# Performance work log

Hardware: AMD Instinct MI355X
Metric: run time of the kernel (lower is better)

The kernel has to match this reference:

```python
import jax, jax.numpy as jnp
import numpy as np

N = 50000   # nodes
E = 640000  # edges (before self-loops)
D = 128     # in_dim == out_dim
H = 4       # heads
C = 32      # per-head channels (out_dim // heads)
ED = 1      # edge_dim
NEG_SLOPE = 0.2
LN_EPS = 1e-5


def setup_inputs() -> dict:
    key = jax.random.key(0)
    ks = jax.random.split(key, 8)
    glorot = lambda k, sh, fan: jax.random.normal(k, sh, jnp.float32) / np.float32(np.sqrt(fan))
    return dict(
        x=jax.random.normal(ks[0], (N, D), jnp.float32),
        edge_index=jax.random.randint(ks[1], (2, E), 0, N, dtype=jnp.int32),
        edge_attr=jax.random.uniform(ks[2], (E, ED), jnp.float32),
        W_l=glorot(ks[3], (D, H * C), D), b_l=jnp.zeros((H * C,), jnp.float32),
        W_r=glorot(ks[4], (D, H * C), D), b_r=jnp.zeros((H * C,), jnp.float32),
        W_e=glorot(ks[5], (ED, H * C), ED),
        att=glorot(ks[6], (H, C), C),
        bias=jnp.zeros((H * C,), jnp.float32),
        ln_gamma=jnp.ones((H * C,), jnp.float32),
        ln_beta=jnp.zeros((H * C,), jnp.float32),
    )


def reference(x, edge_index, edge_attr, W_l, b_l, W_r, b_r, W_e, att, bias, ln_gamma, ln_beta):
    n = x.shape[0]
    src, dst = edge_index[0], edge_index[1]
    # --- add self loops; self-loop edge_attr = mean of incoming attrs (PyG fill_value='mean') ---
    attr_sum = jax.ops.segment_sum(edge_attr, dst, num_segments=n)          # (N, ED)
    cnt = jax.ops.segment_sum(jnp.ones((edge_attr.shape[0], 1), edge_attr.dtype), dst, num_segments=n)
    loop_attr = attr_sum / jnp.maximum(cnt, 1.0)
    ea = jnp.concatenate([edge_attr, loop_attr], axis=0)                    # (E+N, ED)
    loop = jnp.arange(n, dtype=src.dtype)
    src = jnp.concatenate([src, loop])
    dst = jnp.concatenate([dst, loop])
    # --- GATv2: separate source/target linear transforms ---
    x_l = (x @ W_l + b_l).reshape(n, H, C)   # source (x_j)
    x_r = (x @ W_r + b_r).reshape(n, H, C)   # target (x_i)
    e_f = (ea @ W_e).reshape(-1, H, C)       # edge embedding (E+N, H, C)
    xj = x_l[src]                            # gather (E+N, H, C)
    m = jax.nn.leaky_relu(xj + x_r[dst] + e_f, NEG_SLOPE)
    alpha = jnp.einsum('ehc,hc->eh', m, att)
    # --- segment softmax over incoming edges of each target node ---
    amax = jax.ops.segment_max(alpha, dst, num_segments=n)  # every node has a self-loop
    ex = jnp.exp(alpha - amax[dst])
    denom = jax.ops.segment_sum(ex, dst, num_segments=n)
    a = ex / denom[dst]                                     # (E+N, H); attn dropout is eval no-op
    # --- scatter-aggregate messages, concat heads, conv bias ---
    out = jax.ops.segment_sum(xj * a[..., None], dst, num_segments=n).reshape(n, H * C) + bias
    # --- ELU, dropout (eval no-op), residual (in_dim == out_dim, no res_proj), LayerNorm ---
    out = jax.nn.elu(out) + x
    mu = jnp.mean(out, axis=-1, keepdims=True)
    var = jnp.var(out, axis=-1, keepdims=True)
    return (out - mu) * jax.lax.rsqrt(var + LN_EPS) * ln_gamma + ln_beta
```

## Files before the change

kernel.cpp:

```cpp
#include <hip/hip_runtime.h>
#include <hip/hip_fp16.h>
#include <math.h>

#define DCH 128
#define NEG 0.2f
#define LOG2E 1.44269504088896f
#define NPART 256
#define RCAP 2512
#define BCAP 1152

typedef _Float16 f16x8 __attribute__((ext_vector_type(8)));
typedef float    f32x4 __attribute__((ext_vector_type(4)));

static __device__ __forceinline__ float dpp_radd4(float v) {
    int b;
    b = __builtin_amdgcn_update_dpp(0, __float_as_int(v), 0xB1, 0xF, 0xF, true);
    v += __int_as_float(b);
    b = __builtin_amdgcn_update_dpp(0, __float_as_int(v), 0x4E, 0xF, 0xF, true);
    v += __int_as_float(b);
    return v;
}

__global__ __launch_bounds__(256) void k_prep(
        const float* __restrict__ x, __half* __restrict__ xf16, int total4,
        const float* __restrict__ Wl, const float* __restrict__ Wr,
        __half* __restrict__ wtl, __half* __restrict__ wtr, int nb_cvt) {
    int bid = blockIdx.x;
    if (bid < nb_cvt) {
        int i = bid * 256 + (int)threadIdx.x;
        if (i >= total4) return;
        float4 v = ((const float4*)x)[i];
        __half2* dst = (__half2*)xf16 + 2 * (size_t)i;
        dst[0] = __floats2half2_rn(v.x, v.y);
        dst[1] = __floats2half2_rn(v.z, v.w);
    } else {
        int t = (bid - nb_cvt) * 256 + (int)threadIdx.x;
        if (t >= 2 * DCH * DCH) return;
        const float* W = (t < DCH * DCH) ? Wl : Wr;
        __half* wt = (t < DCH * DCH) ? wtl : wtr;
        int u = t & (DCH * DCH - 1);
        int k = u >> 7, j = u & 127;
        wt[j * 128 + k] = __float2half_rn(W[u]);
    }
}

__global__ __launch_bounds__(256) void k_mmpart(
        const __half* __restrict__ xf16,
        const __half* __restrict__ wtl, const __half* __restrict__ wtr,
        const float* __restrict__ bl, const float* __restrict__ br,
        __half* __restrict__ xl16, float* __restrict__ xro, int N,
        const int* __restrict__ ei, const float* __restrict__ eattr,
        unsigned* __restrict__ sorted, unsigned* __restrict__ cnt,
        unsigned* __restrict__ gbase,
        int E, int NB, int chunkE, int nb_mm) {
    if ((int)blockIdx.x >= nb_mm) {
        __shared__ unsigned lcnt[1024];
        __shared__ unsigned lbase[1024];
        __shared__ unsigned lcur[1024];
        __shared__ unsigned recbuf[RCAP];
        __shared__ unsigned wsum2[4], wpre2[5];
        int p = (int)blockIdx.x - nb_mm;
        int t = threadIdx.x, lane = t & 63, w = t >> 6;
        for (int i = t; i < 1024; i += 256) lcnt[i] = 0u;
        __syncthreads();
        int e0 = p * chunkE;
        int e1 = e0 + chunkE; if (e1 > E) e1 = E;
        for (int e = e0 + t; e < e1; e += 256)
            atomicAdd(&lcnt[ei[E + e] >> 6], 1u);
        __syncthreads();
        unsigned c0 = lcnt[t * 4 + 0], c1 = lcnt[t * 4 + 1];
        unsigned c2 = lcnt[t * 4 + 2], c3 = lcnt[t * 4 + 3];
        unsigned s4 = c0 + c1 + c2 + c3;
        unsigned sc = s4;
        #pragma unroll
        for (int o = 1; o < 64; o <<= 1) {
            unsigned tmp = __shfl_up(sc, o, 64);
            if (lane >= o) sc += tmp;
        }
        if (lane == 63) wsum2[w] = sc;
        __syncthreads();
        if (t == 0) {
            wpre2[0] = 0;
            #pragma unroll
            for (int k = 0; k < 4; ++k) wpre2[k + 1] = wpre2[k] + wsum2[k];
        }
        __syncthreads();
        unsigned base4 = wpre2[w] + sc - s4;
        lbase[t * 4 + 0] = base4;
        lbase[t * 4 + 1] = base4 + c0;
        lbase[t * 4 + 2] = base4 + c0 + c1;
        lbase[t * 4 + 3] = base4 + c0 + c1 + c2;
        lcur[t * 4 + 0] = lbase[t * 4 + 0];
        lcur[t * 4 + 1] = lbase[t * 4 + 1];
        lcur[t * 4 + 2] = lbase[t * 4 + 2];
        lcur[t * 4 + 3] = lbase[t * 4 + 3];
        __syncthreads();
        unsigned gB = (unsigned)(p * chunkE);
        for (int b = t; b < NB; b += 256) {
            cnt[(size_t)b * NPART + p] = lcnt[b];
            gbase[(size_t)b * NPART + p] = gB + lbase[b];
        }
        for (int e = e0 + t; e < e1; e += 256) {
            int d = ei[E + e], s = ei[e];
            float a = eattr[e];
            int b = d >> 6, dl = d & 63;
            unsigned qq = (unsigned)fminf(a * 1024.f + 0.5f, 1023.f);
            unsigned rank = atomicAdd(&lcur[b], 1u);
            if (rank < RCAP)
                recbuf[rank] = (unsigned)dl | ((unsigned)s << 6) | (qq << 22);
        }
        __syncthreads();
        int tot = e1 - e0;
        for (int i = t; i < tot; i += 256)
            sorted[(size_t)p * chunkE + i] = recbuf[i];
        return;
    }
    int wave = threadIdx.x >> 6, lane = threadIdx.x & 63;
    int node0 = blockIdx.x * 64;
    int jbase = wave * 32;
    int rl = lane & 15, kg = lane >> 4;
    f32x4 acc[4][2][2];
    #pragma unroll
    for (int a = 0; a < 4; ++a)
        #pragma unroll
        for (int b = 0; b < 2; ++b)
            #pragma unroll
            for (int c = 0; c < 2; ++c)
                acc[a][b][c] = (f32x4){0.f, 0.f, 0.f, 0.f};
    #pragma unroll
    for (int ks = 0; ks < 4; ++ks) {
        int koff = ks * 32 + kg * 8;
        f16x8 av[4];
        #pragma unroll
        for (int rt = 0; rt < 4; ++rt) {
            int row = node0 + rt * 16 + rl;
            if (row >= N) row = N - 1;
            av[rt] = *(const f16x8*)(xf16 + (size_t)row * 128 + koff);
        }
        #pragma unroll
        for (int jt = 0; jt < 2; ++jt) {
            int j = jbase + jt * 16 + rl;
            size_t ob = (size_t)j * 128 + koff;
            f16x8 bL = *(const f16x8*)(wtl + ob);
            f16x8 bR = *(const f16x8*)(wtr + ob);
            #pragma unroll
            for (int rt = 0; rt < 4; ++rt) {
                acc[rt][jt][0] = __builtin_amdgcn_mfma_f32_16x16x32_f16(av[rt], bL, acc[rt][jt][0], 0, 0, 0);
                acc[rt][jt][1] = __builtin_amdgcn_mfma_f32_16x16x32_f16(av[rt], bR, acc[rt][jt][1], 0, 0, 0);
            }
        }
    }
    float blv[2], brv[2];
    #pragma unroll
    for (int jt = 0; jt < 2; ++jt) {
        int j = jbase + jt * 16 + rl;
        blv[jt] = bl[j]; brv[jt] = br[j];
    }
    #pragma unroll
    for (int rt = 0; rt < 4; ++rt) {
        #pragma unroll
        for (int r = 0; r < 4; ++r) {
            int row = node0 + rt * 16 + kg * 4 + r;
            if (row < N) {
                #pragma unroll
                for (int jt = 0; jt < 2; ++jt) {
                    int j = jbase + jt * 16 + rl;
                    xl16[(size_t)row * 128 + j] = __float2half_rn(acc[rt][jt][0][r] + blv[jt]);
                    xro[(size_t)row * 128 + j] = acc[rt][jt][1][r] + brv[jt];
                }
            }
        }
    }
}

__global__ __launch_bounds__(256) void k_fill2(
        const unsigned* __restrict__ sorted, const unsigned* __restrict__ cnt,
        const unsigned* __restrict__ gbase,
        unsigned* __restrict__ csr, uint2* __restrict__ ndesc,
        float* __restrict__ lattr, int N) {
    __shared__ unsigned lraw[BCAP];
    __shared__ unsigned hcnt[64], qsum[64];
    __shared__ unsigned wsum[4], wpre[5];
    __shared__ int ncur[64];
    __shared__ int tot_s;
    int t = threadIdx.x, lane = t & 63, w = t >> 6;
    int bucket = blockIdx.x;
    if (t < 64) { hcnt[t] = 0u; qsum[t] = 0u; }
    unsigned v = cnt[(size_t)bucket * NPART + t];
    unsigned gb = gbase[(size_t)bucket * NPART + t];
    int sc = (int)v;
    #pragma unroll
    for (int o = 1; o < 64; o <<= 1) {
        int tmp = __shfl_up(sc, o, 64);
        if (lane >= o) sc += tmp;
    }
    if (lane == 63) wsum[w] = (unsigned)sc;
    __syncthreads();
    if (t == 0) {
        wpre[0] = 0;
        #pragma unroll
        for (int k = 0; k < 4; ++k) wpre[k + 1] = wpre[k] + wsum[k];
        tot_s = (int)(wpre[4] < BCAP ? wpre[4] : BCAP);
    }
    __syncthreads();
    unsigned sb = wpre[w] + (unsigned)sc - v;
    {
        const unsigned* src = sorted + gb;
        for (int i = 0; i < (int)v; ++i) {
            unsigned idx = sb + (unsigned)i;
            if (idx < BCAP) {
                unsigned rec = src[i];
                lraw[idx] = rec;
                int dl = (int)(rec & 63u);
                atomicAdd(&hcnt[dl], 1u);
                atomicAdd(&qsum[dl], rec >> 22);
            }
        }
    }
    __syncthreads();
    if (t < 64) {
        int nv = (int)hcnt[t], nsc = nv;
        #pragma unroll
        for (int o = 1; o < 64; o <<= 1) {
            int tmp = __shfl_up(nsc, o, 64);
            if (t >= o) nsc += tmp;
        }
        int nb = nsc - nv;
        ncur[t] = nb;
        int node = bucket * 64 + t;
        if (node < N) {
            ndesc[node] = make_uint2((unsigned)(bucket * BCAP + nb), (unsigned)nv);
            lattr[node] = ((float)qsum[t] * (1.f / 1024.f)) / fmaxf((float)nv, 1.f);
        }
    }
    __syncthreads();
    int tot = tot_s;
    for (int i = t; i < tot; i += 256) {
        unsigned rec = lraw[i];
        int dl = (int)(rec & 63u);
        int pos = atomicAdd(&ncur[dl], 1);
        csr[(size_t)bucket * BCAP + pos] = ((rec >> 6) & 0xFFFFu) | ((rec >> 22) << 16);
    }
}

__global__ __launch_bounds__(256) void k_gat(
        const __half* __restrict__ xl16, const float* __restrict__ xrp, const float* __restrict__ x,
        const unsigned* __restrict__ csr, const uint2* __restrict__ ndesc,
        const float* __restrict__ lattr,
        const float* __restrict__ We, const float* __restrict__ att, const float* __restrict__ bias,
        const float* __restrict__ gamma, const float* __restrict__ beta,
        float* __restrict__ out, int N) {
    int wid = threadIdx.x >> 6;
    int lane = threadIdx.x & 63;
    int node = blockIdx.x * 4 + wid;
    if (node >= N) return;
    int q = lane >> 4;
    int sl = lane & 15;
    int c8 = sl << 3;

    float4 attA = *(const float4*)(att + c8);
    float4 attB = *(const float4*)(att + c8 + 4);
    attA.x *= LOG2E; attA.y *= LOG2E; attA.z *= LOG2E; attA.w *= LOG2E;
    attB.x *= LOG2E; attB.y *= LOG2E; attB.z *= LOG2E; attB.w *= LOG2E;
    float4 weA = *(const float4*)(We + c8);
    float4 weB = *(const float4*)(We + c8 + 4);
    float4 xrA = *(const float4*)(xrp + (size_t)node * 128 + c8);
    float4 xrB = *(const float4*)(xrp + (size_t)node * 128 + c8 + 4);

    uint2 nd = ndesc[node];
    int beg = (int)nd.x, deg = (int)nd.y;
    float la = lattr[node];
    int T = deg + 1;

    float4 accA = {0.f, 0.f, 0.f, 0.f}, accB = {0.f, 0.f, 0.f, 0.f};
    float den = 0.f;

    auto meta = [&](int pp, int& ss, float& ea, float& vm) {
        int idx = pp + q;
        bool real = idx < deg;
        unsigned rec = real ? csr[beg + idx] : 0u;
        ss = real ? (int)(rec & 0xFFFFu) : node;
        ea = real ? (float)(rec >> 16) * (1.f / 1024.f) : la;
        vm = (idx <= deg) ? 1.f : 0.f;
    };
    auto gth = [&](int ss) -> uint4 {
        return *(const uint4*)(xl16 + ((size_t)ss << 7) + c8);
    };

    int sA, sB, sC, sD;
    float eaA, eaB, eaC, eaD, vA, vB, vC, vD;
    uint4 gA4, gB4, gC4;
    meta(0, sA, eaA, vA);
    meta(4, sB, eaB, vB);
    meta(8, sC, eaC, vC);
    meta(12, sD, eaD, vD);
    gA4 = gth(sA); gB4 = gth(sB); gC4 = gth(sC);

    for (int p = 0; p < T; p += 4) {
        float2 g0 = __half22float2(*(const __half2*)&gA4.x);
        float2 g1 = __half22float2(*(const __half2*)&gA4.y);
        float2 g2 = __half22float2(*(const __half2*)&gA4.z);
        float2 g3 = __half22float2(*(const __half2*)&gA4.w);
        float t0 = g0.x + fmaf(eaA, weA.x, xrA.x); t0 = fmaxf(t0, t0 * NEG);
        float t1 = g0.y + fmaf(eaA, weA.y, xrA.y); t1 = fmaxf(t1, t1 * NEG);
        float t2 = g1.x + fmaf(eaA, weA.z, xrA.z); t2 = fmaxf(t2, t2 * NEG);
        float t3 = g1.y + fmaf(eaA, weA.w, xrA.w); t3 = fmaxf(t3, t3 * NEG);
        float t4 = g2.x + fmaf(eaA, weB.x, xrB.x); t4 = fmaxf(t4, t4 * NEG);
        float t5 = g2.y + fmaf(eaA, weB.y, xrB.y); t5 = fmaxf(t5, t5 * NEG);
        float t6 = g3.x + fmaf(eaA, weB.z, xrB.z); t6 = fmaxf(t6, t6 * NEG);
        float t7 = g3.y + fmaf(eaA, weB.w, xrB.w); t7 = fmaxf(t7, t7 * NEG);
        float d = t0 * attA.x;
        d = fmaf(t1, attA.y, d); d = fmaf(t2, attA.z, d); d = fmaf(t3, attA.w, d);
        d = fmaf(t4, attB.x, d); d = fmaf(t5, attB.y, d); d = fmaf(t6, attB.z, d);
        d = fmaf(t7, attB.w, d);
        float pt = dpp_radd4(d);
        float pe = exp2f(pt) * vA;
        den += pe;
        accA.x = fmaf(pe, g0.x, accA.x); accA.y = fmaf(pe, g0.y, accA.y);
        accA.z = fmaf(pe, g1.x, accA.z); accA.w = fmaf(pe, g1.y, accA.w);
        accB.x = fmaf(pe, g2.x, accB.x); accB.y = fmaf(pe, g2.y, accB.y);
        accB.z = fmaf(pe, g3.x, accB.z); accB.w = fmaf(pe, g3.y, accB.w);
        eaA = eaB; vA = vB; gA4 = gB4;
        eaB = eaC; vB = vC; gB4 = gC4;
        sC = sD; eaC = eaD; vC = vD;
        gC4 = gth(sC);
        meta(p + 16, sD, eaD, vD);
    }

    den += __shfl_xor(den, 16, 64);
    accA.x += __shfl_xor(accA.x, 16, 64); accA.y += __shfl_xor(accA.y, 16, 64);
    accA.z += __shfl_xor(accA.z, 16, 64); accA.w += __shfl_xor(accA.w, 16, 64);
    accB.x += __shfl_xor(accB.x, 16, 64); accB.y += __shfl_xor(accB.y, 16, 64);
    accB.z += __shfl_xor(accB.z, 16, 64); accB.w += __shfl_xor(accB.w, 16, 64);
    den += __shfl_xor(den, 32, 64);
    accA.x += __shfl_xor(accA.x, 32, 64); accA.y += __shfl_xor(accA.y, 32, 64);
    accA.z += __shfl_xor(accA.z, 32, 64); accA.w += __shfl_xor(accA.w, 32, 64);
    accB.x += __shfl_xor(accB.x, 32, 64); accB.y += __shfl_xor(accB.y, 32, 64);
    accB.z += __shfl_xor(accB.z, 32, 64); accB.w += __shfl_xor(accB.w, 32, 64);

    float inv = 1.f / den;
    float4 biA = *(const float4*)(bias + c8);
    float4 biB = *(const float4*)(bias + c8 + 4);
    float o0 = fmaf(accA.x, inv, biA.x), o1 = fmaf(accA.y, inv, biA.y);
    float o2 = fmaf(accA.z, inv, biA.z), o3 = fmaf(accA.w, inv, biA.w);
    float o4 = fmaf(accB.x, inv, biB.x), o5 = fmaf(accB.y, inv, biB.y);
    float o6 = fmaf(accB.z, inv, biB.z), o7 = fmaf(accB.w, inv, biB.w);
    o0 = o0 > 0.f ? o0 : (__expf(o0) - 1.f);
    o1 = o1 > 0.f ? o1 : (__expf(o1) - 1.f);
    o2 = o2 > 0.f ? o2 : (__expf(o2) - 1.f);
    o3 = o3 > 0.f ? o3 : (__expf(o3) - 1.f);
    o4 = o4 > 0.f ? o4 : (__expf(o4) - 1.f);
    o5 = o5 > 0.f ? o5 : (__expf(o5) - 1.f);
    o6 = o6 > 0.f ? o6 : (__expf(o6) - 1.f);
    o7 = o7 > 0.f ? o7 : (__expf(o7) - 1.f);
    float4 xvA = *(const float4*)(x + (size_t)node * 128 + c8);
    float4 xvB = *(const float4*)(x + (size_t)node * 128 + c8 + 4);
    o0 += xvA.x; o1 += xvA.y; o2 += xvA.z; o3 += xvA.w;
    o4 += xvB.x; o5 += xvB.y; o6 += xvB.z; o7 += xvB.w;
    float r1 = ((o0 + o1) + (o2 + o3)) + ((o4 + o5) + (o6 + o7));
    float r2 = o0 * o0;
    r2 = fmaf(o1, o1, r2); r2 = fmaf(o2, o2, r2); r2 = fmaf(o3, o3, r2);
    r2 = fmaf(o4, o4, r2); r2 = fmaf(o5, o5, r2); r2 = fmaf(o6, o6, r2);
    r2 = fmaf(o7, o7, r2);
    #pragma unroll
    for (int mk = 1; mk < 16; mk <<= 1) {
        r1 += __shfl_xor(r1, mk, 16);
        r2 += __shfl_xor(r2, mk, 16);
    }
    float mean = r1 * (1.f / 128.f);
    float var  = r2 * (1.f / 128.f) - mean * mean;
    float rr = rsqrtf(var + 1e-5f);
    if (q == 0) {
        float4 gmA = *(const float4*)(gamma + c8);
        float4 gmB = *(const float4*)(gamma + c8 + 4);
        float4 btA = *(const float4*)(beta + c8);
        float4 btB = *(const float4*)(beta + c8 + 4);
        float4 wA, wB;
        wA.x = (o0 - mean) * rr * gmA.x + btA.x;
        wA.y = (o1 - mean) * rr * gmA.y + btA.y;
        wA.z = (o2 - mean) * rr * gmA.z + btA.z;
        wA.w = (o3 - mean) * rr * gmA.w + btA.w;
        wB.x = (o4 - mean) * rr * gmB.x + btB.x;
        wB.y = (o5 - mean) * rr * gmB.y + btB.y;
        wB.z = (o6 - mean) * rr * gmB.z + btB.z;
        wB.w = (o7 - mean) * rr * gmB.w + btB.w;
        *(float4*)(out + (size_t)node * 128 + c8) = wA;
        *(float4*)(out + (size_t)node * 128 + c8 + 4) = wB;
    }
}

extern "C" void kernel_launch(void* const* d_in, const int* in_sizes, int n_in,
                              void* d_out, int out_size, void* d_ws, size_t ws_size,
                              hipStream_t stream) {
    const float* x     = (const float*)d_in[0];
    const int*   ei    = (const int*)d_in[1];
    const float* eattr = (const float*)d_in[2];
    const float* Wl    = (const float*)d_in[3];
    const float* bl    = (const float*)d_in[4];
    const float* Wr    = (const float*)d_in[5];
    const float* br    = (const float*)d_in[6];
    const float* We    = (const float*)d_in[7];
    const float* att   = (const float*)d_in[8];
    const float* bias  = (const float*)d_in[9];
    const float* gam   = (const float*)d_in[10];
    const float* bet   = (const float*)d_in[11];
    float* out = (float*)d_out;
    int N = in_sizes[0] / DCH;
    int E = in_sizes[1] / 2;
    int NB = (N + 63) / 64;

    char* base = (char*)d_ws;
    size_t off = 0;
    auto alloc = [&](size_t nbytes) -> void* {
        void* p = base + off;
        off += (nbytes + 255) & ~(size_t)255;
        return p;
    };
    int chunkE = (E + NPART - 1) / NPART;
    unsigned* sorted = (unsigned*)alloc((size_t)NPART * chunkE * 4);
    unsigned* cnt    = (unsigned*)alloc((size_t)NB * NPART * 4);
    unsigned* gbase  = (unsigned*)alloc((size_t)NB * NPART * 4);
    unsigned* csr    = (unsigned*)alloc((size_t)NB * BCAP * 4);
    uint2*    ndesc  = (uint2*)alloc((size_t)N * 8);
    float*    lattr  = (float*)alloc((size_t)N * 4);
    __half*   xl16   = (__half*)alloc((size_t)N * DCH * 2);
    float*    xrb    = (float*)alloc((size_t)N * DCH * 4);
    __half*   xf16   = (__half*)alloc((size_t)N * DCH * 2);
    __half*   wtl    = (__half*)alloc((size_t)DCH * DCH * 2);
    __half*   wtr    = (__half*)alloc((size_t)DCH * DCH * 2);
    (void)n_in; (void)out_size; (void)ws_size;

    int total4  = N * DCH / 4;
    int nb_cvt  = (total4 + 255) / 256;
    int nb_cvtw = (2 * DCH * DCH + 255) / 256;
    int nb_mm   = (N + 63) / 64;

    k_prep<<<nb_cvt + nb_cvtw, 256, 0, stream>>>(
        x, xf16, total4, Wl, Wr, wtl, wtr, nb_cvt);
    k_mmpart<<<nb_mm + NPART, 256, 0, stream>>>(
        xf16, wtl, wtr, bl, br, xl16, xrb, N,
        ei, eattr, sorted, cnt, gbase, E, NB, chunkE, nb_mm);
    k_fill2<<<NB, 256, 0, stream>>>(
        sorted, cnt, gbase, csr, ndesc, lattr, N);
    k_gat<<<(N + 3) / 4, 256, 0, stream>>>(
        xl16, xrb, x, csr, ndesc, lattr, We, att, bias, gam, bet, out, N);
}
```

Before: 105.9 us.

## Store x_r in fp16, read fp16 residual, simplify gather loop to 8-edge batches

The target projection x_r is now written and read as fp16 instead of fp32, halving its store and load traffic. The residual add reads the fp16 copy of x rather than the fp32 input. The rotating three-deep software-pipelined gather in the attention loop is replaced by a simpler loop that issues two gathers per iteration and then consumes them. This trades precision on x_r and the residual for bandwidth, and may expose more gather latency because prefetch across iterations is gone.

Measured after the change: 114.2 us. 7.9% more time.

```diff
diff --git a/kernel.cpp b/kernel.cpp
--- a/kernel.cpp
+++ b/kernel.cpp
@@ -48,7 +48,7 @@
         const __half* __restrict__ xf16,
         const __half* __restrict__ wtl, const __half* __restrict__ wtr,
         const float* __restrict__ bl, const float* __restrict__ br,
-        __half* __restrict__ xl16, float* __restrict__ xro, int N,
+        __half* __restrict__ xl16, __half* __restrict__ xr16, int N,
         const int* __restrict__ ei, const float* __restrict__ eattr,
         unsigned* __restrict__ sorted, unsigned* __restrict__ cnt,
         unsigned* __restrict__ gbase,
@@ -166,7 +166,7 @@
                 for (int jt = 0; jt < 2; ++jt) {
                     int j = jbase + jt * 16 + rl;
                     xl16[(size_t)row * 128 + j] = __float2half_rn(acc[rt][jt][0][r] + blv[jt]);
-                    xro[(size_t)row * 128 + j] = acc[rt][jt][1][r] + brv[jt];
+                    xr16[(size_t)row * 128 + j] = __float2half_rn(acc[rt][jt][1][r] + brv[jt]);
                 }
             }
         }
@@ -244,7 +244,8 @@
 }
 
 __global__ __launch_bounds__(256) void k_gat(
-        const __half* __restrict__ xl16, const float* __restrict__ xrp, const float* __restrict__ x,
+        const __half* __restrict__ xl16, const __half* __restrict__ xr16,
+        const __half* __restrict__ xf16,
         const unsigned* __restrict__ csr, const uint2* __restrict__ ndesc,
         const float* __restrict__ lattr,
         const float* __restrict__ We, const float* __restrict__ att, const float* __restrict__ bias,
@@ -264,8 +265,11 @@
     attB.x *= LOG2E; attB.y *= LOG2E; attB.z *= LOG2E; attB.w *= LOG2E;
     float4 weA = *(const float4*)(We + c8);
     float4 weB = *(const float4*)(We + c8 + 4);
-    float4 xrA = *(const float4*)(xrp + (size_t)node * 128 + c8);
-    float4 xrB = *(const float4*)(xrp + (size_t)node * 128 + c8 + 4);
+    uint4 xrraw = *(const uint4*)(xr16 + (size_t)node * 128 + c8);
+    float2 xr0 = __half22float2(*(const __half2*)&xrraw.x);
+    float2 xr1 = __half22float2(*(const __half2*)&xrraw.y);
+    float2 xr2 = __half22float2(*(const __half2*)&xrraw.z);
+    float2 xr3 = __half22float2(*(const __half2*)&xrraw.w);
 
     uint2 nd = ndesc[node];
     int beg = (int)nd.x, deg = (int)nd.y;
@@ -283,48 +287,40 @@
         ea = real ? (float)(rec >> 16) * (1.f / 1024.f) : la;
         vm = (idx <= deg) ? 1.f : 0.f;
     };
-    auto gth = [&](int ss) -> uint4 {
-        return *(const uint4*)(xl16 + ((size_t)ss << 7) + c8);
-    };
-
-    int sA, sB, sC, sD;
-    float eaA, eaB, eaC, eaD, vA, vB, vC, vD;
-    uint4 gA4, gB4, gC4;
-    meta(0, sA, eaA, vA);
-    meta(4, sB, eaB, vB);
-    meta(8, sC, eaC, vC);
-    meta(12, sD, eaD, vD);
-    gA4 = gth(sA); gB4 = gth(sB); gC4 = gth(sC);
-
-    for (int p = 0; p < T; p += 4) {
-        float2 g0 = __half22float2(*(const __half2*)&gA4.x);
-        float2 g1 = __half22float2(*(const __half2*)&gA4.y);
-        float2 g2 = __half22float2(*(const __half2*)&gA4.z);
-        float2 g3 = __half22float2(*(const __half2*)&gA4.w);
-        float t0 = g0.x + fmaf(eaA, weA.x, xrA.x); t0 = fmaxf(t0, t0 * NEG);
-        float t1 = g0.y + fmaf(eaA, weA.y, xrA.y); t1 = fmaxf(t1, t1 * NEG);
-        float t2 = g1.x + fmaf(eaA, weA.z, xrA.z); t2 = fmaxf(t2, t2 * NEG);
-        float t3 = g1.y + fmaf(eaA, weA.w, xrA.w); t3 = fmaxf(t3, t3 * NEG);
-        float t4 = g2.x + fmaf(eaA, weB.x, xrB.x); t4 = fmaxf(t4, t4 * NEG);
-        float t5 = g2.y + fmaf(eaA, weB.y, xrB.y); t5 = fmaxf(t5, t5 * NEG);
-        float t6 = g3.x + fmaf(eaA, weB.z, xrB.z); t6 = fmaxf(t6, t6 * NEG);
-        float t7 = g3.y + fmaf(eaA, weB.w, xrB.w); t7 = fmaxf(t7, t7 * NEG);
+    auto consume = [&](uint4 graw, float ea, float vm) {
+        float2 g0 = __half22float2(*(const __half2*)&graw.x);
+        float2 g1 = __half22float2(*(const __half2*)&graw.y);
+        float2 g2 = __half22float2(*(const __half2*)&graw.z);
+        float2 g3 = __half22float2(*(const __half2*)&graw.w);
+        float t0 = g0.x + fmaf(ea, weA.x, xr0.x); t0 = fmaxf(t0, t0 * NEG);
+        float t1 = g0.y + fmaf(ea, weA.y, xr0.y); t1 = fmaxf(t1, t1 * NEG);
+        float t2 = g1.x + fmaf(ea, weA.z, xr1.x); t2 = fmaxf(t2, t2 * NEG);
+        float t3 = g1.y + fmaf(ea, weA.w, xr1.y); t3 = fmaxf(t3, t3 * NEG);
+        float t4 = g2.x + fmaf(ea, weB.x, xr2.x); t4 = fmaxf(t4, t4 * NEG);
+        float t5 = g2.y + fmaf(ea, weB.y, xr2.y); t5 = fmaxf(t5, t5 * NEG);
+        float t6 = g3.x + fmaf(ea, weB.z, xr3.x); t6 = fmaxf(t6, t6 * NEG);
+        float t7 = g3.y + fmaf(ea, weB.w, xr3.y); t7 = fmaxf(t7, t7 * NEG);
         float d = t0 * attA.x;
         d = fmaf(t1, attA.y, d); d = fmaf(t2, attA.z, d); d = fmaf(t3, attA.w, d);
         d = fmaf(t4, attB.x, d); d = fmaf(t5, attB.y, d); d = fmaf(t6, attB.z, d);
         d = fmaf(t7, attB.w, d);
         float pt = dpp_radd4(d);
-        float pe = exp2f(pt) * vA;
+        float pe = exp2f(pt) * vm;
         den += pe;
         accA.x = fmaf(pe, g0.x, accA.x); accA.y = fmaf(pe, g0.y, accA.y);
         accA.z = fmaf(pe, g1.x, accA.z); accA.w = fmaf(pe, g1.y, accA.w);
         accB.x = fmaf(pe, g2.x, accB.x); accB.y = fmaf(pe, g2.y, accB.y);
         accB.z = fmaf(pe, g3.x, accB.z); accB.w = fmaf(pe, g3.y, accB.w);
-        eaA = eaB; vA = vB; gA4 = gB4;
-        eaB = eaC; vB = vC; gB4 = gC4;
-        sC = sD; eaC = eaD; vC = vD;
-        gC4 = gth(sC);
-        meta(p + 16, sD, eaD, vD);
+    };
+
+    for (int p = 0; p < T; p += 8) {
+        int sX, sY; float eaX, eaY, vX, vY;
+        meta(p, sX, eaX, vX);
+        meta(p + 4, sY, eaY, vY);
+        uint4 gX = *(const uint4*)(xl16 + ((size_t)sX << 7) + c8);
+        uint4 gY = *(const uint4*)(xl16 + ((size_t)sY << 7) + c8);
+        consume(gX, eaX, vX);
+        consume(gY, eaY, vY);
     }
 
     den += __shfl_xor(den, 16, 64);
@@ -353,10 +349,13 @@
     o5 = o5 > 0.f ? o5 : (__expf(o5) - 1.f);
     o6 = o6 > 0.f ? o6 : (__expf(o6) - 1.f);
     o7 = o7 > 0.f ? o7 : (__expf(o7) - 1.f);
-    float4 xvA = *(const float4*)(x + (size_t)node * 128 + c8);
-    float4 xvB = *(const float4*)(x + (size_t)node * 128 + c8 + 4);
-    o0 += xvA.x; o1 += xvA.y; o2 += xvA.z; o3 += xvA.w;
-    o4 += xvB.x; o5 += xvB.y; o6 += xvB.z; o7 += xvB.w;
+    uint4 xvraw = *(const uint4*)(xf16 + (size_t)node * 128 + c8);
+    float2 xv0 = __half22float2(*(const __half2*)&xvraw.x);
+    float2 xv1 = __half22float2(*(const __half2*)&xvraw.y);
+    float2 xv2 = __half22float2(*(const __half2*)&xvraw.z);
+    float2 xv3 = __half22float2(*(const __half2*)&xvraw.w);
+    o0 += xv0.x; o1 += xv0.y; o2 += xv1.x; o3 += xv1.y;
+    o4 += xv2.x; o5 += xv2.y; o6 += xv3.x; o7 += xv3.y;
     float r1 = ((o0 + o1) + (o2 + o3)) + ((o4 + o5) + (o6 + o7));
     float r2 = o0 * o0;
     r2 = fmaf(o1, o1, r2); r2 = fmaf(o2, o2, r2); r2 = fmaf(o3, o3, r2);
@@ -424,7 +423,7 @@
     uint2*    ndesc  = (uint2*)alloc((size_t)N * 8);
     float*    lattr  = (float*)alloc((size_t)N * 4);
     __half*   xl16   = (__half*)alloc((size_t)N * DCH * 2);
-    float*    xrb    = (float*)alloc((size_t)N * DCH * 4);
+    __half*   xr16   = (__half*)alloc((size_t)N * DCH * 2);
     __half*   xf16   = (__half*)alloc((size_t)N * DCH * 2);
     __half*   wtl    = (__half*)alloc((size_t)DCH * DCH * 2);
     __half*   wtr    = (__half*)alloc((size_t)DCH * DCH * 2);
@@ -438,10 +437,10 @@
     k_prep<<<nb_cvt + nb_cvtw, 256, 0, stream>>>(
         x, xf16, total4, Wl, Wr, wtl, wtr, nb_cvt);
     k_mmpart<<<nb_mm + NPART, 256, 0, stream>>>(
-        xf16, wtl, wtr, bl, br, xl16, xrb, N,
+        xf16, wtl, wtr, bl, br, xl16, xr16, N,
         ei, eattr, sorted, cnt, gbase, E, NB, chunkE, nb_mm);
     k_fill2<<<NB, 256, 0, stream>>>(
         sorted, cnt, gbase, csr, ndesc, lattr, N);
     k_gat<<<(N + 3) / 4, 256, 0, stream>>>(
-        xl16, xrb, x, csr, ndesc, lattr, We, att, bias, gam, bet, out, N);
-}
+        xl16, xr16, xf16, csr, ndesc, lattr, We, att, bias, gam, bet, out, N);
+}
```
